# Optimization experiments

Hardware: AMD Instinct MI355X
Metric: run time of the kernel (lower is better)

The kernel has to match this reference:

```python
import jax, jax.numpy as jnp
import numpy as np

TEMPERATURE = 100.0  # exponential-smoothing temperature from __init__ default
ETA = 1.0            # feature/label cost tradeoff


def _cdist(a, b):
    # Euclidean distance matrix [M, N] between rows of a [M, D] and b [N, D]
    sq = (jnp.sum(a * a, axis=1)[:, None]
          + jnp.sum(b * b, axis=1)[None, :]
          - 2.0 * (a @ b.T))
    return jnp.sqrt(jnp.maximum(sq, 1e-12))


def setup_inputs() -> dict:
    key = jax.random.key(0)
    ks = jax.random.split(key, 9)
    B, Nt, Ns, H, Wd, C = 1024, 8192, 8192, 32, 32, 10
    D = H * Wd
    x = jax.random.normal(ks[0], (B, H, Wd), jnp.float32)
    target_features = jax.random.normal(ks[1], (Nt, H, Wd), jnp.float32)
    aligned_source_features = jax.random.normal(ks[2], (Nt, H, Wd), jnp.float32)
    source_features = jax.random.normal(ks[3], (Ns, H, Wd), jnp.float32)
    source_high_dim_labels = jax.random.uniform(ks[4], (Ns, C), jnp.float32)
    aligned_target_labels = jax.random.uniform(ks[5], (Ns, C), jnp.float32)
    source_label_distances = jax.random.uniform(ks[6], (C, C), jnp.float32)
    W = jax.random.normal(ks[7], (D, C), jnp.float32) * 0.02
    b = jnp.zeros((C,), jnp.float32)
    return {
        "x": x,
        "target_features": target_features,
        "aligned_source_features": aligned_source_features,
        "source_features": source_features,
        "source_high_dim_labels": source_high_dim_labels,
        "aligned_target_labels": aligned_target_labels,
        "source_label_distances": source_label_distances,
        "W": W,
        "b": b,
    }


def reference(x, target_features, aligned_source_features, source_features,
              source_high_dim_labels, aligned_target_labels,
              source_label_distances, W, b):
    B = x.shape[0]
    xf = x.reshape(B, -1)                                   # [B, D]
    tf = target_features.reshape(target_features.shape[0], -1)       # [Nt, D]
    asf = aligned_source_features.reshape(aligned_source_features.shape[0], -1)  # [Nt, D]
    sf = source_features.reshape(source_features.shape[0], -1)       # [Ns, D]

    # --- feature transport: target -> source (plain_softmax) ---
    d_feat = _cdist(xf, tf)                                 # [B, Nt]
    w_feat = jax.nn.softmax(-TEMPERATURE * d_feat, axis=1)  # [B, Nt]
    x_src = w_feat @ asf                                    # [B, D] in source space

    # --- source model (linear classifier head -> soft predictions) ---
    preds = jax.nn.softmax(x_src @ W + b, axis=1)           # [B, C]

    # --- label transport: source -> target (plain_softmax) ---
    cost = _cdist(x_src, sf)                                # feature_dists=True: [B, Ns]
    # label_dists=True: cost of moving predicted label mass to each sample's label
    cost = cost + ETA * (preds @ source_label_distances @ source_high_dim_labels.T)
    w_lab = jax.nn.softmax(-TEMPERATURE * cost, axis=1)     # [B, Ns]
    y = w_lab @ aligned_target_labels                       # [B, C] in target label space
    return y
```

## Files before the change

### kernel.cpp

```cpp
#include <hip/hip_runtime.h>
#include <hip/hip_bf16.h>
#include <math.h>

#define B_ROWS 1024
#define NT 8192
#define NS 8192
#define DIM 1024
#define NC 10
#define TEMP 100.0f
#define WCAP 1024
#define PREP_RPB 8

typedef __bf16 bf16x8 __attribute__((ext_vector_type(8)));
typedef __bf16 bf16x4 __attribute__((ext_vector_type(4)));
typedef float f32x4 __attribute__((ext_vector_type(4)));

#define GLOAD_LDS(g, l) \
    __builtin_amdgcn_global_load_lds((__attribute__((address_space(1))) void*)(g), \
                                     (__attribute__((address_space(3))) void*)(l), 16, 0, 0)

__device__ inline __bf16 split_hi(float v) { return (__bf16)v; }
__device__ inline __bf16 split_lo(float v) {
    __bf16 h = (__bf16)v;
    return (__bf16)(v - (float)h);
}

__device__ inline float wave_max(float v) {
    #pragma unroll
    for (int off = 32; off > 0; off >>= 1)
        v = fmaxf(v, __shfl_down(v, off, 64));
    return v;
}
__device__ inline float wave_sum(float v) {
    #pragma unroll
    for (int off = 32; off > 0; off >>= 1)
        v += __shfl_down(v, off, 64);
    return v;
}

__global__ __launch_bounds__(256) void k_prep0(const float* __restrict__ x,
                                               const float* __restrict__ tf,
                                               const float* __restrict__ sf,
                                               const float* __restrict__ sld,
                                               const float* __restrict__ shdl,
                                               const float* __restrict__ atl,
                                               __bf16* __restrict__ x2,
                                               __bf16* __restrict__ tf2,
                                               __bf16* __restrict__ sf2,
                                               float* __restrict__ nx_,
                                               float* __restrict__ nt_,
                                               float* __restrict__ ns_,
                                               float* __restrict__ M2Tt,
                                               float* __restrict__ atlt) {
    __shared__ float sred[4][PREP_RPB];
    __shared__ float sldL[NC * NC];
    const int NXB = B_ROWS / PREP_RPB;
    const int NTB = NT / PREP_RPB;
    const int NSB = NS / PREP_RPB;
    int b = blockIdx.x;
    int tid = threadIdx.x;
    if (b < NXB + NTB + NSB) {
        const float* Xp; __bf16* X2p; float* np; int r0;
        if (b < NXB)            { Xp = x;  X2p = x2;  np = nx_; r0 = b * PREP_RPB; }
        else if (b < NXB + NTB) { Xp = tf; X2p = tf2; np = nt_; r0 = (b - NXB) * PREP_RPB; }
        else                    { Xp = sf; X2p = sf2; np = ns_; r0 = (b - NXB - NTB) * PREP_RPB; }
        int c = tid * 4;
        int lane = tid & 63, wid = tid >> 6;
        #pragma unroll
        for (int r = 0; r < PREP_RPB; r++) {
            float4 v = *(const float4*)(Xp + (size_t)(r0 + r) * DIM + c);
            bf16x4 h, l;
            h[0] = split_hi(v.x); l[0] = split_lo(v.x);
            h[1] = split_hi(v.y); l[1] = split_lo(v.y);
            h[2] = split_hi(v.z); l[2] = split_lo(v.z);
            h[3] = split_hi(v.w); l[3] = split_lo(v.w);
            *(bf16x4*)(X2p + (size_t)(r0 + r) * 2048 + c) = h;
            *(bf16x4*)(X2p + (size_t)(r0 + r) * 2048 + 1024 + c) = l;
            float acc = v.x * v.x + v.y * v.y + v.z * v.z + v.w * v.w;
            float w = wave_sum(acc);
            if (lane == 0) sred[wid][r] = w;
        }
        __syncthreads();
        if (tid < PREP_RPB)
            np[r0 + tid] = sred[0][tid] + sred[1][tid] + sred[2][tid] + sred[3][tid];
    } else {
        if (tid < NC * NC) sldL[tid] = sld[tid];
        __syncthreads();
        int j = (b - NXB - NTB - NSB) * 256 + tid;
        float sh[NC], at[NC];
        #pragma unroll
        for (int k = 0; k < NC; k++) sh[k] = shdl[(size_t)j * NC + k];
        #pragma unroll
        for (int c = 0; c < NC; c++) at[c] = atl[(size_t)j * NC + c];
        #pragma unroll
        for (int c = 0; c < NC; c++) {
            float t = 0.f;
            #pragma unroll
            for (int k = 0; k < NC; k++) t += sldL[c * NC + k] * sh[k];
            M2Tt[c * NS + j] = t;
            atlt[c * NS + j] = at[c];
        }
    }
}

template <bool LOGITS>
__global__ __launch_bounds__(512, 4) void k_gemm3(const __bf16* __restrict__ A2,
                                                  const __bf16* __restrict__ B2,
                                                  float* __restrict__ C,
                                                  int M, int N, int K, int ksplit,
                                                  const float* __restrict__ rowN,
                                                  const float* __restrict__ colN) {
    __shared__ unsigned short AhS[8192], AlS[8192], BhS[8192], BlS[8192];
    __shared__ float extraL[LOGITS ? 256 : 2];
    float* rnL = extraL;
    float* cnL = extraL + 128;

    int tid = threadIdx.x;
    int wid = tid >> 6, lane = tid & 63;
    int wm = (wid >> 2) * 64, wn = (wid & 3) * 32;
    int id = blockIdx.y * gridDim.x + blockIdx.x;
    int bn_i = ((id >> 6) << 3) | (id & 7);
    int bm_i = (id >> 3) & 7;
    int bm = bm_i * 128, bn = bn_i * 128;
    size_t K2 = 2 * (size_t)K;
    int k_begin = blockIdx.z * ksplit;
    int nsteps = ksplit >> 6;

    if (LOGITS) {
        if (tid < 128) rnL[tid] = rowN[bm + tid];
        else if (tid < 256) cnL[tid - 128] = colN[bn + tid - 128];
    }

    f32x4 acc[4][2];
    #pragma unroll
    for (int i = 0; i < 4; i++)
        #pragma unroll
        for (int j = 0; j < 2; j++) acc[i][j] = (f32x4){0.f, 0.f, 0.f, 0.f};

    int arr = wid & 3, hh = wid >> 2;
    char* arrB = (arr == 0) ? (char*)AhS : (arr == 1) ? (char*)AlS
               : (arr == 2) ? (char*)BhS : (char*)BlS;
    const __bf16* gbase = (arr < 2) ? A2 : B2;
    int rbase = (arr < 2) ? bm : bn;
    int hilo = (arr & 1) ? K : 0;
    int r_in = lane >> 3;
    int cgo = ((lane & 7) ^ r_in) * 8;
    const __bf16* gw = gbase + (size_t)(rbase + hh * 64 + r_in) * K2 + hilo + k_begin + cgo;
    int ldst = hh * 8192;
    size_t row8 = 8 * K2;

    int ra = lane & 15, q = lane >> 4;
    int aoff[4][2], boff[2][2];
    #pragma unroll
    for (int kh = 0; kh < 2; kh++) {
        #pragma unroll
        for (int i = 0; i < 4; i++) {
            int chunk = ((kh << 2) | q) ^ (ra & 7);
            aoff[i][kh] = (wm + i * 16 + ra) * 64 + chunk * 8;
        }
        #pragma unroll
        for (int j = 0; j < 2; j++) {
            int chunk = ((kh << 2) | q) ^ (ra & 7);
            boff[j][kh] = (wn + j * 16 + ra) * 64 + chunk * 8;
        }
    }
    const __bf16* AhE = (const __bf16*)AhS;
    const __bf16* AlE = (const __bf16*)AlS;
    const __bf16* BhE = (const __bf16*)BhS;
    const __bf16* BlE = (const __bf16*)BlS;

    for (int ks = 0; ks < nsteps; ks++) {
        __syncthreads();
        #pragma unroll
        for (int p = 0; p < 8; p++) {
            GLOAD_LDS(gw + (size_t)p * row8, arrB + ldst + p * 1024);
        }
        gw += 64;
        __syncthreads();

        #pragma unroll
        for (int kh = 0; kh < 2; kh++) {
            bf16x8 ah[4], al[4];
            #pragma unroll
            for (int mi = 0; mi < 4; mi++) {
                ah[mi] = *(const bf16x8*)(AhE + aoff[mi][kh]);
                al[mi] = *(const bf16x8*)(AlE + aoff[mi][kh]);
            }
            #pragma unroll
            for (int ni = 0; ni < 2; ni++) {
                bf16x8 bh = *(const bf16x8*)(BhE + boff[ni][kh]);
                bf16x8 bl = *(const bf16x8*)(BlE + boff[ni][kh]);
                #pragma unroll
                for (int mi = 0; mi < 4; mi++) {
                    acc[mi][ni] = __builtin_amdgcn_mfma_f32_16x16x32_bf16(ah[mi], bh, acc[mi][ni], 0, 0, 0);
                    acc[mi][ni] = __builtin_amdgcn_mfma_f32_16x16x32_bf16(ah[mi], bl, acc[mi][ni], 0, 0, 0);
                    acc[mi][ni] = __builtin_amdgcn_mfma_f32_16x16x32_bf16(al[mi], bh, acc[mi][ni], 0, 0, 0);
                }
            }
        }
    }

    if (!LOGITS) {
        float* Cb = C + (size_t)blockIdx.z * M * N;
        #pragma unroll
        for (int mi = 0; mi < 4; mi++) {
            #pragma unroll
            for (int ni = 0; ni < 2; ni++) {
                int r0 = bm + wm + mi * 16 + q * 4;
                int c0 = bn + wn + ni * 16 + ra;
                Cb[(size_t)(r0 + 0) * N + c0] = acc[mi][ni][0];
                Cb[(size_t)(r0 + 1) * N + c0] = acc[mi][ni][1];
                Cb[(size_t)(r0 + 2) * N + c0] = acc[mi][ni][2];
                Cb[(size_t)(r0 + 3) * N + c0] = acc[mi][ni][3];
            }
        }
    } else {
        #pragma unroll
        for (int mi = 0; mi < 4; mi++) {
            #pragma unroll
            for (int ni = 0; ni < 2; ni++) {
                int cl = wn + ni * 16 + ra;
                float cn = cnL[cl];
                #pragma unroll
                for (int i = 0; i < 4; i++) {
                    int rl = wm + mi * 16 + q * 4 + i;
                    float sq = rnL[rl] + cn - 2.f * acc[mi][ni][i];
                    float d = sqrtf(fmaxf(sq, 1e-12f));
                    C[(size_t)(bm + rl) * N + bn + cl] = -TEMP * d;
                }
            }
        }
    }
}

__global__ __launch_bounds__(256) void k_xsrc(const float* __restrict__ S,
                                              const float* __restrict__ asf,
                                              const float* __restrict__ W,
                                              const float* __restrict__ bias,
                                              __bf16* __restrict__ xsrc2,
                                              float* __restrict__ nx2_,
                                              float* __restrict__ preds) {
    __shared__ float sm[4];
    __shared__ float ss[4];
    __shared__ int   sidx[WCAP];
    __shared__ float swt[WCAP];
    __shared__ int   scnt;
    __shared__ float red[4][NC + 1];
    int row = blockIdx.x;
    int tid = threadIdx.x;
    int lane = tid & 63, wid = tid >> 6;
    if (tid == 0) scnt = 0;
    const float4* sr = (const float4*)(S + (size_t)row * NT);
    float4 vals[NT / 1024];
    float lmax = -1e30f;
    #pragma unroll
    for (int u = 0; u < NT / 1024; u++) {
        float4 v = sr[tid + u * 256];
        vals[u] = v;
        lmax = fmaxf(fmaxf(fmaxf(v.x, v.y), fmaxf(v.z, v.w)), lmax);
    }
    float wmx = wave_max(lmax);
    if (lane == 0) sm[wid] = wmx;
    __syncthreads();
    float bmax = fmaxf(fmaxf(sm[0], sm[1]), fmaxf(sm[2], sm[3]));
    float lsum = 0.f;
    #pragma unroll
    for (int u = 0; u < NT / 1024; u++) {
        float4 v = vals[u];
        v.x = __expf(v.x - bmax); v.y = __expf(v.y - bmax);
        v.z = __expf(v.z - bmax); v.w = __expf(v.w - bmax);
        vals[u] = v;
        lsum += v.x + v.y + v.z + v.w;
    }
    float wsv = wave_sum(lsum);
    if (lane == 0) ss[wid] = wsv;
    __syncthreads();
    float bsum = ss[0] + ss[1] + ss[2] + ss[3];
    float inv = 1.0f / bsum;
    float thr = 1e-8f * bsum;
    #pragma unroll
    for (int u = 0; u < NT / 1024; u++) {
        float4 v = vals[u];
        int j = (tid + u * 256) * 4;
        if (v.x > thr) { int k = atomicAdd(&scnt, 1); if (k < WCAP) { sidx[k] = j;     swt[k] = v.x * inv; } }
        if (v.y > thr) { int k = atomicAdd(&scnt, 1); if (k < WCAP) { sidx[k] = j + 1; swt[k] = v.y * inv; } }
        if (v.z > thr) { int k = atomicAdd(&scnt, 1); if (k < WCAP) { sidx[k] = j + 2; swt[k] = v.z * inv; } }
        if (v.w > thr) { int k = atomicAdd(&scnt, 1); if (k < WCAP) { sidx[k] = j + 3; swt[k] = v.w * inv; } }
    }
    __syncthreads();
    int cnt = scnt < WCAP ? scnt : WCAP;
    int c = tid * 4;
    float sx = 0.f, sy = 0.f, sz = 0.f, sw = 0.f;
    for (int i = 0; i < cnt; i++) {
        float wg = swt[i];
        float4 v = *(const float4*)(asf + (size_t)sidx[i] * DIM + c);
        sx += wg * v.x; sy += wg * v.y; sz += wg * v.z; sw += wg * v.w;
    }
    bf16x4 h, l;
    h[0] = split_hi(sx); l[0] = split_lo(sx);
    h[1] = split_hi(sy); l[1] = split_lo(sy);
    h[2] = split_hi(sz); l[2] = split_lo(sz);
    h[3] = split_hi(sw); l[3] = split_lo(sw);
    *(bf16x4*)(xsrc2 + (size_t)row * 2048 + c) = h;
    *(bf16x4*)(xsrc2 + (size_t)row * 2048 + 1024 + c) = l;
    float accn = sx * sx + sy * sy + sz * sz + sw * sw;
    float accp[NC];
    #pragma unroll
    for (int cc = 0; cc < NC; cc++)
        accp[cc] = sx * W[(c + 0) * NC + cc] + sy * W[(c + 1) * NC + cc]
                 + sz * W[(c + 2) * NC + cc] + sw * W[(c + 3) * NC + cc];
    accn = wave_sum(accn);
    #pragma unroll
    for (int cc = 0; cc < NC; cc++) accp[cc] = wave_sum(accp[cc]);
    if (lane == 0) {
        red[wid][0] = accn;
        #pragma unroll
        for (int cc = 0; cc < NC; cc++) red[wid][1 + cc] = accp[cc];
    }
    __syncthreads();
    if (tid == 0) {
        nx2_[row] = red[0][0] + red[1][0] + red[2][0] + red[3][0];
        float lo[NC];
        float m = -1e30f;
        #pragma unroll
        for (int cc = 0; cc < NC; cc++) {
            lo[cc] = red[0][1 + cc] + red[1][1 + cc] + red[2][1 + cc] + red[3][1 + cc]
                   + bias[cc];
            m = fmaxf(m, lo[cc]);
        }
        float ssum = 0.f;
        #pragma unroll
        for (int cc = 0; cc < NC; cc++) {
            lo[cc] = __expf(lo[cc] - m);
            ssum += lo[cc];
        }
        float iv = 1.0f / ssum;
        #pragma unroll
        for (int cc = 0; cc < NC; cc++) preds[(size_t)row * NC + cc] = lo[cc] * iv;
    }
}

__global__ __launch_bounds__(256) void k_lab_softmax_y(const float* __restrict__ S,
                                                       const float* __restrict__ predsG,
                                                       const float* __restrict__ M2Tt,
                                                       const float* __restrict__ atlt,
                                                       float* __restrict__ y) {
    int r0 = blockIdx.x * 2, r1 = r0 + 1;
    float pr0[NC], pr1[NC];
    #pragma unroll
    for (int c = 0; c < NC; c++) {
        pr0[c] = TEMP * predsG[(size_t)r0 * NC + c];
        pr1[c] = TEMP * predsG[(size_t)r1 * NC + c];
    }
    const float4* s0 = (const float4*)(S + (size_t)r0 * NS);
    const float4* s1 = (const float4*)(S + (size_t)r1 * NS);
    const float4* M2 = (const float4*)M2Tt;
    const float4* AT = (const float4*)atlt;
    float4 v0[NS / 1024], v1[NS / 1024];
    float m0 = -1e30f, m1 = -1e30f;
    #pragma unroll
    for (int u = 0; u < NS / 1024; u++) {
        int j4 = threadIdx.x + u * 256;
        float4 a = s0[j4], b = s1[j4];
        float4 lab0 = make_float4(0.f, 0.f, 0.f, 0.f);
        float4 lab1 = make_float4(0.f, 0.f, 0.f, 0.f);
        #pragma unroll
        for (int c = 0; c < NC; c++) {
            float4 mv = M2[c * 2048 + j4];
            lab0.x += pr0[c] * mv.x; lab0.y += pr0[c] * mv.y;
            lab0.z += pr0[c] * mv.z; lab0.w += pr0[c] * mv.w;
            lab1.x += pr1[c] * mv.x; lab1.y += pr1[c] * mv.y;
            lab1.z += pr1[c] * mv.z; lab1.w += pr1[c] * mv.w;
        }
        a.x -= lab0.x; a.y -= lab0.y;
        a.z -= lab0.z; a.w -= lab0.w;
        b.x -= lab1.x; b.y -= lab1.y;
        b.z -= lab1.z; b.w -= lab1.w;
        v0[u] = a; v1[u] = b;
        m0 = fmaxf(m0, fmaxf(fmaxf(a.x, a.y), fmaxf(a.z, a.w)));
        m1 = fmaxf(m1, fmaxf(fmaxf(b.x, b.y), fmaxf(b.z, b.w)));
    }
    __shared__ float sm[2][4];
    __shared__ float ss[2][4];
    __shared__ float yred[4][2][NC];
    int lane = threadIdx.x & 63, wid = threadIdx.x >> 6;
    float wm0 = wave_max(m0), wm1 = wave_max(m1);
    if (lane == 0) { sm[0][wid] = wm0; sm[1][wid] = wm1; }
    __syncthreads();
    float bm0 = fmaxf(fmaxf(sm[0][0], sm[0][1]), fmaxf(sm[0][2], sm[0][3]));
    float bm1 = fmaxf(fmaxf(sm[1][0], sm[1][1]), fmaxf(sm[1][2], sm[1][3]));
    float ls0 = 0.f, ls1 = 0.f;
    #pragma unroll
    for (int u = 0; u < NS / 1024; u++) {
        float4 a = v0[u], b = v1[u];
        a.x = __expf(a.x - bm0); a.y = __expf(a.y - bm0);
        a.z = __expf(a.z - bm0); a.w = __expf(a.w - bm0);
        b.x = __expf(b.x - bm1); b.y = __expf(b.y - bm1);
        b.z = __expf(b.z - bm1); b.w = __expf(b.w - bm1);
        v0[u] = a; v1[u] = b;
        ls0 += a.x + a.y + a.z + a.w;
        ls1 += b.x + b.y + b.z + b.w;
    }
    float ws0 = wave_sum(ls0), ws1 = wave_sum(ls1);
    if (lane == 0) { ss[0][wid] = ws0; ss[1][wid] = ws1; }
    __syncthreads();
    float inv0 = 1.0f / (ss[0][0] + ss[0][1] + ss[0][2] + ss[0][3]);
    float inv1 = 1.0f / (ss[1][0] + ss[1][1] + ss[1][2] + ss[1][3]);
    float y0[NC] = {}, y1[NC] = {};
    #pragma unroll
    for (int u = 0; u < NS / 1024; u++) {
        int j4 = threadIdx.x + u * 256;
        float4 a = v0[u], b = v1[u];
        #pragma unroll
        for (int c = 0; c < NC; c++) {
            float4 av = AT[c * 2048 + j4];
            y0[c] += a.x * av.x + a.y * av.y + a.z * av.z + a.w * av.w;
            y1[c] += b.x * av.x + b.y * av.y + b.z * av.z + b.w * av.w;
        }
    }
    #pragma unroll
    for (int c = 0; c < NC; c++) {
        y0[c] = wave_sum(y0[c]) * inv0;
        y1[c] = wave_sum(y1[c]) * inv1;
    }
    if (lane == 0) {
        #pragma unroll
        for (int c = 0; c < NC; c++) { yred[wid][0][c] = y0[c]; yred[wid][1][c] = y1[c]; }
    }
    __syncthreads();
    if (threadIdx.x < 2 * NC) {
        int r = threadIdx.x / NC, c = threadIdx.x - r * NC;
        y[(size_t)(r0 + r) * NC + c] = yred[0][r][c] + yred[1][r][c] + yred[2][r][c] + yred[3][r][c];
    }
}

extern "C" void kernel_launch(void* const* d_in, const int* in_sizes, int n_in,
                              void* d_out, int out_size, void* d_ws, size_t ws_size,
                              hipStream_t stream) {
    const float* x    = (const float*)d_in[0];
    const float* tf   = (const float*)d_in[1];
    const float* asf  = (const float*)d_in[2];
    const float* sf   = (const float*)d_in[3];
    const float* shdl = (const float*)d_in[4];
    const float* atl  = (const float*)d_in[5];
    const float* sld  = (const float*)d_in[6];
    const float* W    = (const float*)d_in[7];
    const float* bias = (const float*)d_in[8];
    float* y = (float*)d_out;

    char* wsb = (char*)d_ws;
    float*  S     = (float*)(wsb);
    __bf16* tf2   = (__bf16*)(wsb + (32u << 20));
    __bf16* sf2   = (__bf16*)(wsb + (64u << 20));
    __bf16* x2    = (__bf16*)(wsb + (96u << 20));
    __bf16* xsrc2 = (__bf16*)(wsb + (100u << 20));
    float*  nt_   = (float*)(wsb + (108u << 20));
    float*  ns_   = nt_ + NT;
    float*  nx_   = ns_ + NS;
    float*  nx2_  = nx_ + B_ROWS;
    float*  preds = nx2_ + B_ROWS;
    float*  M2Tt  = preds + B_ROWS * NC;
    float*  atlt  = M2Tt + NS * NC;

    {
        int nblk = B_ROWS / PREP_RPB + NT / PREP_RPB + NS / PREP_RPB + NS / 256;
        k_prep0<<<nblk, 256, 0, stream>>>(x, tf, sf, sld, shdl, atl,
                                          x2, tf2, sf2, nx_, nt_, ns_, M2Tt, atlt);
    }

    {
        dim3 g(NT / 128, B_ROWS / 128, 1);
        k_gemm3<true><<<g, 512, 0, stream>>>(x2, tf2, S, B_ROWS, NT, DIM, DIM,
                                             nx_, nt_);
    }

    k_xsrc<<<B_ROWS, 256, 0, stream>>>(S, asf, W, bias, xsrc2, nx2_, preds);

    {
        dim3 g(NS / 128, B_ROWS / 128, 1);
        k_gemm3<true><<<g, 512, 0, stream>>>(xsrc2, sf2, S, B_ROWS, NS, DIM, DIM,
                                             nx2_, ns_);
    }
    k_lab_softmax_y<<<B_ROWS / 2, 256, 0, stream>>>(S, preds, M2Tt, atlt, y);
}
```

Baseline: 272.1 us.

## Fuse partial softmax stats and candidate selection into first distance GEMM epilogue

The first distance GEMM no longer writes the full B×Nt logit matrix. Instead each tile computes per-row partial max and sum, and appends columns within a log-threshold of the tile max to a per-row candidate list using atomics. k_xsrc then merges the 64 partial (max, sum) pairs and filters candidates rather than rereading 32 MB of logits. This removes a large global write and read, at the cost of atomics in the epilogue, a capped candidate buffer that could drop entries, and a slightly looser tile-local threshold.

```diff
diff --git a/kernel.cpp b/kernel.cpp
--- a/kernel.cpp
+++ b/kernel.cpp
@@ -9,6 +9,8 @@
 #define NC 10
 #define TEMP 100.0f
 #define WCAP 1024
+#define CCAP 512
+#define LTHR 18.421681f
 #define PREP_RPB 8
 
 typedef __bf16 bf16x8 __attribute__((ext_vector_type(8)));
@@ -36,6 +38,9 @@
     for (int off = 32; off > 0; off >>= 1)
         v += __shfl_down(v, off, 64);
     return v;
+}
+__device__ inline float max4(float4 v) {
+    return fmaxf(fmaxf(v.x, v.y), fmaxf(v.z, v.w));
 }
 
 __global__ __launch_bounds__(256) void k_prep0(const float* __restrict__ x,
@@ -51,7 +56,8 @@
                                                float* __restrict__ nt_,
                                                float* __restrict__ ns_,
                                                float* __restrict__ M2Tt,
-                                               float* __restrict__ atlt) {
+                                               float* __restrict__ atlt,
+                                               int* __restrict__ cnt) {
     __shared__ float sred[4][PREP_RPB];
     __shared__ float sldL[NC * NC];
     const int NXB = B_ROWS / PREP_RPB;
@@ -84,6 +90,10 @@
         if (tid < PREP_RPB)
             np[r0 + tid] = sred[0][tid] + sred[1][tid] + sred[2][tid] + sred[3][tid];
     } else {
+        if (b == NXB + NTB + NSB) {
+            #pragma unroll
+            for (int z = 0; z < 4; z++) cnt[tid + z * 256] = 0;
+        }
         if (tid < NC * NC) sldL[tid] = sld[tid];
         __syncthreads();
         int j = (b - NXB - NTB - NSB) * 256 + tid;
@@ -103,15 +113,15 @@
     }
 }
 
-template <bool LOGITS>
-__global__ __launch_bounds__(512, 4) void k_gemm3(const __bf16* __restrict__ A2,
-                                                  const __bf16* __restrict__ B2,
-                                                  float* __restrict__ C,
-                                                  int M, int N, int K, int ksplit,
-                                                  const float* __restrict__ rowN,
-                                                  const float* __restrict__ colN) {
+
+__global__ __launch_bounds__(512, 4) void k_gemm3L(const __bf16* __restrict__ A2,
+                                                   const __bf16* __restrict__ B2,
+                                                   float* __restrict__ C,
+                                                   int N, int K,
+                                                   const float* __restrict__ rowN,
+                                                   const float* __restrict__ colN) {
     __shared__ unsigned short AhS[8192], AlS[8192], BhS[8192], BlS[8192];
-    __shared__ float extraL[LOGITS ? 256 : 2];
+    __shared__ float extraL[256];
     float* rnL = extraL;
     float* cnL = extraL + 128;
 
@@ -123,13 +133,10 @@
     int bm_i = (id >> 3) & 7;
     int bm = bm_i * 128, bn = bn_i * 128;
     size_t K2 = 2 * (size_t)K;
-    int k_begin = blockIdx.z * ksplit;
-    int nsteps = ksplit >> 6;
-
-    if (LOGITS) {
-        if (tid < 128) rnL[tid] = rowN[bm + tid];
-        else if (tid < 256) cnL[tid - 128] = colN[bn + tid - 128];
-    }
+    int nsteps = K >> 6;
+
+    if (tid < 128) rnL[tid] = rowN[bm + tid];
+    else if (tid < 256) cnL[tid - 128] = colN[bn + tid - 128];
 
     f32x4 acc[4][2];
     #pragma unroll
@@ -145,7 +152,7 @@
     int hilo = (arr & 1) ? K : 0;
     int r_in = lane >> 3;
     int cgo = ((lane & 7) ^ r_in) * 8;
-    const __bf16* gw = gbase + (size_t)(rbase + hh * 64 + r_in) * K2 + hilo + k_begin + cgo;
+    const __bf16* gw = gbase + (size_t)(rbase + hh * 64 + r_in) * K2 + hilo + cgo;
     int ldst = hh * 8192;
     size_t row8 = 8 * K2;
 
@@ -172,12 +179,10 @@
     for (int ks = 0; ks < nsteps; ks++) {
         __syncthreads();
         #pragma unroll
-        for (int p = 0; p < 8; p++) {
+        for (int p = 0; p < 8; p++)
             GLOAD_LDS(gw + (size_t)p * row8, arrB + ldst + p * 1024);
-        }
         gw += 64;
         __syncthreads();
-
         #pragma unroll
         for (int kh = 0; kh < 2; kh++) {
             bf16x8 ah[4], al[4];
@@ -200,40 +205,187 @@
         }
     }
 
-    if (!LOGITS) {
-        float* Cb = C + (size_t)blockIdx.z * M * N;
-        #pragma unroll
-        for (int mi = 0; mi < 4; mi++) {
+    #pragma unroll
+    for (int mi = 0; mi < 4; mi++) {
+        #pragma unroll
+        for (int ni = 0; ni < 2; ni++) {
+            int cl = wn + ni * 16 + ra;
+            float cn = cnL[cl];
+            #pragma unroll
+            for (int i = 0; i < 4; i++) {
+                int rl = wm + mi * 16 + q * 4 + i;
+                float sq = rnL[rl] + cn - 2.f * acc[mi][ni][i];
+                float d = sqrtf(fmaxf(sq, 1e-12f));
+                C[(size_t)(bm + rl) * N + bn + cl] = -TEMP * d;
+            }
+        }
+    }
+}
+
+__global__ __launch_bounds__(512, 4) void k_gemm_part(const __bf16* __restrict__ A2,
+                                                      const __bf16* __restrict__ B2,
+                                                      int N, int K,
+                                                      const float* __restrict__ rowN,
+                                                      const float* __restrict__ colN,
+                                                      float2* __restrict__ ms,
+                                                      int* __restrict__ cnt,
+                                                      int* __restrict__ candj,
+                                                      float* __restrict__ candl) {
+    __shared__ unsigned short AhS[8192], AlS[8192], BhS[8192], BlS[8192];
+    __shared__ float extraL[256];
+    __shared__ float mred[128][4];
+    __shared__ float sredL[128][4];
+    float* rnL = extraL;
+    float* cnL = extraL + 128;
+
+    int tid = threadIdx.x;
+    int wid = tid >> 6, lane = tid & 63;
+    int wm = (wid >> 2) * 64, wn = (wid & 3) * 32;
+    int id = blockIdx.y * gridDim.x + blockIdx.x;
+    int bn_i = ((id >> 6) << 3) | (id & 7);
+    int bm_i = (id >> 3) & 7;
+    int bm = bm_i * 128, bn = bn_i * 128;
+    size_t K2 = 2 * (size_t)K;
+    int nsteps = K >> 6;
+
+    if (tid < 128) rnL[tid] = rowN[bm + tid];
+    else if (tid < 256) cnL[tid - 128] = colN[bn + tid - 128];
+
+    f32x4 acc[4][2];
+    #pragma unroll
+    for (int i = 0; i < 4; i++)
+        #pragma unroll
+        for (int j = 0; j < 2; j++) acc[i][j] = (f32x4){0.f, 0.f, 0.f, 0.f};
+
+    int arr = wid & 3, hh = wid >> 2;
+    char* arrB = (arr == 0) ? (char*)AhS : (arr == 1) ? (char*)AlS
+               : (arr == 2) ? (char*)BhS : (char*)BlS;
+    const __bf16* gbase = (arr < 2) ? A2 : B2;
+    int rbase = (arr < 2) ? bm : bn;
+    int hilo = (arr & 1) ? K : 0;
+    int r_in = lane >> 3;
+    int cgo = ((lane & 7) ^ r_in) * 8;
+    const __bf16* gw = gbase + (size_t)(rbase + hh * 64 + r_in) * K2 + hilo + cgo;
+    int ldst = hh * 8192;
+    size_t row8 = 8 * K2;
+
+    int ra = lane & 15, q = lane >> 4;
+    int aoff[4][2], boff[2][2];
+    #pragma unroll
+    for (int kh = 0; kh < 2; kh++) {
+        #pragma unroll
+        for (int i = 0; i < 4; i++) {
+            int chunk = ((kh << 2) | q) ^ (ra & 7);
+            aoff[i][kh] = (wm + i * 16 + ra) * 64 + chunk * 8;
+        }
+        #pragma unroll
+        for (int j = 0; j < 2; j++) {
+            int chunk = ((kh << 2) | q) ^ (ra & 7);
+            boff[j][kh] = (wn + j * 16 + ra) * 64 + chunk * 8;
+        }
+    }
+    const __bf16* AhE = (const __bf16*)AhS;
+    const __bf16* AlE = (const __bf16*)AlS;
+    const __bf16* BhE = (const __bf16*)BhS;
+    const __bf16* BlE = (const __bf16*)BlS;
+
+    for (int ks = 0; ks < nsteps; ks++) {
+        __syncthreads();
+        #pragma unroll
+        for (int p = 0; p < 8; p++)
+            GLOAD_LDS(gw + (size_t)p * row8, arrB + ldst + p * 1024);
+        gw += 64;
+        __syncthreads();
+        #pragma unroll
+        for (int kh = 0; kh < 2; kh++) {
+            bf16x8 ah[4], al[4];
+            #pragma unroll
+            for (int mi = 0; mi < 4; mi++) {
+                ah[mi] = *(const bf16x8*)(AhE + aoff[mi][kh]);
+                al[mi] = *(const bf16x8*)(AlE + aoff[mi][kh]);
+            }
             #pragma unroll
             for (int ni = 0; ni < 2; ni++) {
-                int r0 = bm + wm + mi * 16 + q * 4;
-                int c0 = bn + wn + ni * 16 + ra;
-                Cb[(size_t)(r0 + 0) * N + c0] = acc[mi][ni][0];
-                Cb[(size_t)(r0 + 1) * N + c0] = acc[mi][ni][1];
-                Cb[(size_t)(r0 + 2) * N + c0] = acc[mi][ni][2];
-                Cb[(size_t)(r0 + 3) * N + c0] = acc[mi][ni][3];
-            }
-        }
-    } else {
-        #pragma unroll
-        for (int mi = 0; mi < 4; mi++) {
+                bf16x8 bh = *(const bf16x8*)(BhE + boff[ni][kh]);
+                bf16x8 bl = *(const bf16x8*)(BlE + boff[ni][kh]);
+                #pragma unroll
+                for (int mi = 0; mi < 4; mi++) {
+                    acc[mi][ni] = __builtin_amdgcn_mfma_f32_16x16x32_bf16(ah[mi], bh, acc[mi][ni], 0, 0, 0);
+                    acc[mi][ni] = __builtin_amdgcn_mfma_f32_16x16x32_bf16(ah[mi], bl, acc[mi][ni], 0, 0, 0);
+                    acc[mi][ni] = __builtin_amdgcn_mfma_f32_16x16x32_bf16(al[mi], bh, acc[mi][ni], 0, 0, 0);
+                }
+            }
+        }
+    }
+
+    float lv[4][2][4];
+    #pragma unroll
+    for (int mi = 0; mi < 4; mi++) {
+        #pragma unroll
+        for (int ni = 0; ni < 2; ni++) {
+            float cn = cnL[wn + ni * 16 + ra];
+            #pragma unroll
+            for (int i = 0; i < 4; i++) {
+                int rl = wm + mi * 16 + q * 4 + i;
+                float sq = rnL[rl] + cn - 2.f * acc[mi][ni][i];
+                lv[mi][ni][i] = -TEMP * sqrtf(fmaxf(sq, 1e-12f));
+            }
+        }
+    }
+    int cw = wid & 3;
+    #pragma unroll
+    for (int mi = 0; mi < 4; mi++) {
+        #pragma unroll
+        for (int i = 0; i < 4; i++) {
+            float v = fmaxf(lv[mi][0][i], lv[mi][1][i]);
+            #pragma unroll
+            for (int off = 1; off < 16; off <<= 1)
+                v = fmaxf(v, __shfl_xor(v, off, 64));
+            float p = __expf(lv[mi][0][i] - v) + __expf(lv[mi][1][i] - v);
+            #pragma unroll
+            for (int off = 1; off < 16; off <<= 1)
+                p += __shfl_xor(p, off, 64);
+            if (ra == 0) {
+                int rl = wm + mi * 16 + q * 4 + i;
+                mred[rl][cw] = v;
+                sredL[rl][cw] = p;
+            }
+        }
+    }
+    __syncthreads();
+    if (tid < 128) {
+        float4 mv = *(const float4*)mred[tid];
+        float m = max4(mv);
+        float4 sv = *(const float4*)sredL[tid];
+        float s = sv.x * __expf(mv.x - m) + sv.y * __expf(mv.y - m)
+                + sv.z * __expf(mv.z - m) + sv.w * __expf(mv.w - m);
+        ms[(size_t)(bm + tid) * 64 + bn_i] = make_float2(m, s);
+    }
+    #pragma unroll
+    for (int mi = 0; mi < 4; mi++) {
+        #pragma unroll
+        for (int i = 0; i < 4; i++) {
+            int rl = wm + mi * 16 + q * 4 + i;
+            float thr = max4(*(const float4*)mred[rl]) - LTHR;
             #pragma unroll
             for (int ni = 0; ni < 2; ni++) {
-                int cl = wn + ni * 16 + ra;
-                float cn = cnL[cl];
-                #pragma unroll
-                for (int i = 0; i < 4; i++) {
-                    int rl = wm + mi * 16 + q * 4 + i;
-                    float sq = rnL[rl] + cn - 2.f * acc[mi][ni][i];
-                    float d = sqrtf(fmaxf(sq, 1e-12f));
-                    C[(size_t)(bm + rl) * N + bn + cl] = -TEMP * d;
+                if (lv[mi][ni][i] > thr) {
+                    int gr = bm + rl;
+                    int k = atomicAdd(&cnt[gr], 1);
+                    if (k < CCAP) {
+                        candj[(size_t)gr * CCAP + k] = bn + wn + ni * 16 + ra;
+                        candl[(size_t)gr * CCAP + k] = lv[mi][ni][i];
+                    }
                 }
             }
         }
     }
 }
 
-__global__ __launch_bounds__(256) void k_xsrc(const float* __restrict__ S,
+__global__ __launch_bounds__(256) void k_xsrc(const float2* __restrict__ ms,
+                                              const int* __restrict__ cnt,
+                                              const int* __restrict__ candj,
+                                              const float* __restrict__ candl,
                                               const float* __restrict__ asf,
                                               const float* __restrict__ W,
                                               const float* __restrict__ bias,
@@ -250,48 +402,29 @@
     int tid = threadIdx.x;
     int lane = tid & 63, wid = tid >> 6;
     if (tid == 0) scnt = 0;
-    const float4* sr = (const float4*)(S + (size_t)row * NT);
-    float4 vals[NT / 1024];
-    float lmax = -1e30f;
-    #pragma unroll
-    for (int u = 0; u < NT / 1024; u++) {
-        float4 v = sr[tid + u * 256];
-        vals[u] = v;
-        lmax = fmaxf(fmaxf(fmaxf(v.x, v.y), fmaxf(v.z, v.w)), lmax);
-    }
-    float wmx = wave_max(lmax);
+    float2 msv = ms[(size_t)row * 64 + lane];
+    float wmx = wave_max(msv.x);
     if (lane == 0) sm[wid] = wmx;
     __syncthreads();
-    float bmax = fmaxf(fmaxf(sm[0], sm[1]), fmaxf(sm[2], sm[3]));
-    float lsum = 0.f;
-    #pragma unroll
-    for (int u = 0; u < NT / 1024; u++) {
-        float4 v = vals[u];
-        v.x = __expf(v.x - bmax); v.y = __expf(v.y - bmax);
-        v.z = __expf(v.z - bmax); v.w = __expf(v.w - bmax);
-        vals[u] = v;
-        lsum += v.x + v.y + v.z + v.w;
-    }
-    float wsv = wave_sum(lsum);
+    float M = fmaxf(fmaxf(sm[0], sm[1]), fmaxf(sm[2], sm[3]));
+    float sp = msv.y * __expf(msv.x - M);
+    float wsv = wave_sum(sp);
     if (lane == 0) ss[wid] = wsv;
     __syncthreads();
-    float bsum = ss[0] + ss[1] + ss[2] + ss[3];
-    float inv = 1.0f / bsum;
-    float thr = 1e-8f * bsum;
-    #pragma unroll
-    for (int u = 0; u < NT / 1024; u++) {
-        float4 v = vals[u];
-        int j = (tid + u * 256) * 4;
-        if (v.x > thr) { int k = atomicAdd(&scnt, 1); if (k < WCAP) { sidx[k] = j;     swt[k] = v.x * inv; } }
-        if (v.y > thr) { int k = atomicAdd(&scnt, 1); if (k < WCAP) { sidx[k] = j + 1; swt[k] = v.y * inv; } }
-        if (v.z > thr) { int k = atomicAdd(&scnt, 1); if (k < WCAP) { sidx[k] = j + 2; swt[k] = v.z * inv; } }
-        if (v.w > thr) { int k = atomicAdd(&scnt, 1); if (k < WCAP) { sidx[k] = j + 3; swt[k] = v.w * inv; } }
-    }
-    __syncthreads();
-    int cnt = scnt < WCAP ? scnt : WCAP;
+    float inv = 1.0f / ss[0];
+    int n = cnt[row]; n = n < CCAP ? n : CCAP;
+    for (int i = tid; i < n; i += 256) {
+        float w = __expf(candl[(size_t)row * CCAP + i] - M) * inv;
+        if (w > 1e-8f) {
+            int k = atomicAdd(&scnt, 1);
+            if (k < WCAP) { sidx[k] = candj[(size_t)row * CCAP + i]; swt[k] = w; }
+        }
+    }
+    __syncthreads();
+    int cw = scnt < WCAP ? scnt : WCAP;
     int c = tid * 4;
     float sx = 0.f, sy = 0.f, sz = 0.f, sw = 0.f;
-    for (int i = 0; i < cnt; i++) {
+    for (int i = 0; i < cw; i++) {
         float wg = swt[i];
         float4 v = *(const float4*)(asf + (size_t)sidx[i] * DIM + c);
         sx += wg * v.x; sy += wg * v.y; sz += wg * v.z; sw += wg * v.w;
@@ -449,6 +582,10 @@
     float* y = (float*)d_out;
 
     char* wsb = (char*)d_ws;
+    int*    candj = (int*)(wsb);
+    float*  candl = (float*)(wsb + (2u << 20));
+    float2* ms    = (float2*)(wsb + (4u << 20));
+    int*    cnt   = (int*)(wsb + (4u << 20) + (512u << 10));
     float*  S     = (float*)(wsb);
     __bf16* tf2   = (__bf16*)(wsb + (32u << 20));
     __bf16* sf2   = (__bf16*)(wsb + (64u << 20));
@@ -465,21 +602,22 @@
     {
         int nblk = B_ROWS / PREP_RPB + NT / PREP_RPB + NS / PREP_RPB + NS / 256;
         k_prep0<<<nblk, 256, 0, stream>>>(x, tf, sf, sld, shdl, atl,
-                                          x2, tf2, sf2, nx_, nt_, ns_, M2Tt, atlt);
+                                          x2, tf2, sf2, nx_, nt_, ns_, M2Tt, atlt,
+                                          cnt);
     }
 
     {
         dim3 g(NT / 128, B_ROWS / 128, 1);
-        k_gemm3<true><<<g, 512, 0, stream>>>(x2, tf2, S, B_ROWS, NT, DIM, DIM,
-                                             nx_, nt_);
-    }
-
-    k_xsrc<<<B_ROWS, 256, 0, stream>>>(S, asf, W, bias, xsrc2, nx2_, preds);
+        k_gemm_part<<<g, 512, 0, stream>>>(x2, tf2, NT, DIM, nx_, nt_,
+                                           ms, cnt, candj, candl);
+    }
+
+    k_xsrc<<<B_ROWS, 256, 0, stream>>>(ms, cnt, candj, candl, asf, W, bias,
+                                       xsrc2, nx2_, preds);
 
     {
         dim3 g(NS / 128, B_ROWS / 128, 1);
-        k_gemm3<true><<<g, 512, 0, stream>>>(xsrc2, sf2, S, B_ROWS, NS, DIM, DIM,
-                                             nx2_, ns_);
+        k_gemm3L<<<g, 512, 0, stream>>>(xsrc2, sf2, S, NS, DIM, nx2_, ns_);
     }
     k_lab_softmax_y<<<B_ROWS / 2, 256, 0, stream>>>(S, preds, M2Tt, atlt, y);
 }
```

Measured after the change: 304.8 us. +12.0%, slower.
